# Kernel tuning notes

Measured on AMD Instinct MI355X. Metric: run time of the kernel, lower is better.

## Reference

```python
import jax, jax.numpy as jnp
import numpy as np

B, L, K, S, D, H, C = 32, 256, 50, 16, 128, 4, 128
V, NN, NU, NS = 50000, 100000, 50000, 5000


def mha(q, k, v, in_w, in_b, out_w, out_b, n_heads):
    # PyTorch nn.MultiheadAttention (batch_first, eval mode) semantics.
    d = q.shape[-1]
    hd = d // n_heads
    wq, wk, wv = jnp.split(in_w, 3, axis=0)
    bq, bk, bv = jnp.split(in_b, 3)
    def heads(t):
        return t.reshape(t.shape[:-1] + (n_heads, hd))
    qh = heads(q @ wq.T + bq)
    kh = heads(k @ wk.T + bk)
    vh = heads(v @ wv.T + bv)
    scores = jnp.einsum('...qhd,...khd->...hqk', qh, kh) / jnp.sqrt(jnp.asarray(hd, q.dtype))
    attn = jax.nn.softmax(scores, axis=-1)
    o = jnp.einsum('...hqk,...khd->...qhd', attn, vh)
    o = o.reshape(o.shape[:-2] + (d,))
    return o @ out_w.T + out_b


def conv1d(x, w, b):
    # x: [B, D, L], w: [Cout, D, k]
    y = jax.lax.conv_general_dilated(x, w, (1,), 'VALID', dimension_numbers=('NCH', 'OIH', 'NCH'))
    return y + b[None, :, None]


def meta_path_module(paths, gru_wih, gru_whh, gru_bih, gru_bhh, in_w, in_b, out_w, out_b, ln_g, ln_b):
    # paths: [B, S, T, D] -> [B, D]
    b, s, t, d = paths.shape
    x = paths.reshape(b * s, t, d)
    def step(h, xt):
        gi = xt @ gru_wih.T + gru_bih
        gh = h @ gru_whh.T + gru_bhh
        ir, iz, inn = jnp.split(gi, 3, axis=-1)
        hr, hz, hn = jnp.split(gh, 3, axis=-1)
        r = jax.nn.sigmoid(ir + hr)
        z = jax.nn.sigmoid(iz + hz)
        n = jnp.tanh(inn + r * hn)
        return (1.0 - z) * n + z * h, None
    h0 = jnp.zeros((b * s, d), paths.dtype)
    h, _ = jax.lax.scan(step, h0, jnp.swapaxes(x, 0, 1))
    enc = h.reshape(b, s, d)
    attn = mha(enc, enc, enc, in_w, in_b, out_w, out_b, H)
    y = enc + attn
    mu = jnp.mean(y, -1, keepdims=True)
    var = jnp.var(y, -1, keepdims=True)
    y = (y - mu) / jnp.sqrt(var + 1e-5) * ln_g + ln_b
    return jnp.mean(y, axis=1)


def _forward(word_table, news_table, user_table, source_table,
             wa_in_w, wa_in_b, wa_out_w, wa_out_b,
             conv_w3, conv_b3, conv_w4, conv_b4, conv_w5, conv_b5, fc_w, fc_b,
             nsn_gru_wih, nsn_gru_whh, nsn_gru_bih, nsn_gru_bhh,
             nsn_in_w, nsn_in_b, nsn_out_w, nsn_out_b, nsn_ln_g, nsn_ln_b,
             nun_gru_wih, nun_gru_whh, nun_gru_bih, nun_gru_bhh,
             nun_in_w, nun_in_b, nun_out_w, nun_out_b, nun_ln_g, nun_ln_b,
             mp_w1, mp_b1, mp_w2, mp_b2, cls_w1, cls_b1, cls_w2, cls_b2,
             news_ids, news_word_indices, word_ctx_ids, nsn_src, nsn_end, nun_usr, nun_end):
    # --- fine-grained word embeds: per-token query attending over context news ---
    base = word_table[news_word_indices]              # [B, L, D]
    ctx = news_table[word_ctx_ids]                    # [B, L, K, D] (dominant gather)
    q = base[:, :, None, :]                           # [B, L, 1, D]
    fine = mha(q, ctx, ctx, wa_in_w, wa_in_b, wa_out_w, wa_out_b, H)[:, :, 0, :]
    pad = (news_word_indices == 0)[..., None]
    doc = jnp.where(pad, jnp.zeros((), base.dtype), fine)   # padding_idx=0 -> zeros
    # --- coarse CNN encoder ---
    x = jnp.swapaxes(doc, 1, 2)                       # [B, D, L]
    pooled = [jnp.max(jax.nn.relu(conv1d(x, w, b)), axis=2)
              for w, b in ((conv_w3, conv_b3), (conv_w4, conv_b4), (conv_w5, conv_b5))]
    semantic = jnp.concatenate(pooled, axis=1) @ fc_w.T + fc_b   # [B, D]
    # --- meta-path interaction ---
    start = jnp.broadcast_to(news_table[news_ids][:, None, :], (B, S, D))
    nsn_paths = jnp.stack([start, source_table[nsn_src], news_table[nsn_end]], axis=2)
    nun_paths = jnp.stack([start, user_table[nun_usr], news_table[nun_end]], axis=2)
    nsn_e = meta_path_module(nsn_paths, nsn_gru_wih, nsn_gru_whh, nsn_gru_bih, nsn_gru_bhh,
                             nsn_in_w, nsn_in_b, nsn_out_w, nsn_out_b, nsn_ln_g, nsn_ln_b)
    nun_e = meta_path_module(nun_paths, nun_gru_wih, nun_gru_whh, nun_gru_bih, nun_gru_bhh,
                             nun_in_w, nun_in_b, nun_out_w, nun_out_b, nun_ln_g, nun_ln_b)
    stack = jnp.stack([nsn_e, nun_e], axis=1)         # [B, 2, D]
    sc = jnp.tanh(stack @ mp_w1.T + mp_b1) @ mp_w2.T + mp_b2
    w = jax.nn.softmax(sc, axis=1)
    struct = jnp.sum(stack * w, axis=1)
    comb = jnp.concatenate([semantic, struct], axis=1)
    hcls = jax.nn.relu(comb @ cls_w1.T + cls_b1)
    return hcls @ cls_w2.T + cls_b2                   # [B, 2]


def setup_inputs() -> dict:
    key = jax.random.key(0)
    ks = iter(jax.random.split(key, 80))
    def p(shape):
        return (jax.random.normal(next(ks), shape, jnp.float32) * 0.02)
    inp = {}
    inp['news_ids'] = jax.random.randint(next(ks), (B,), 0, NN)
    inp['news_word_indices'] = jax.random.randint(next(ks), (B, L), 0, V)
    inp['word_ctx_ids'] = jax.random.randint(next(ks), (B, L, K), 0, NN)
    inp['nsn_src'] = jax.random.randint(next(ks), (B, S), 0, NS)
    inp['nsn_end'] = jax.random.randint(next(ks), (B, S), 0, NN)
    inp['nun_usr'] = jax.random.randint(next(ks), (B, S), 0, NU)
    inp['nun_end'] = jax.random.randint(next(ks), (B, S), 0, NN)
    inp['word_table'] = p((V, D)).at[0].set(0.0)
    inp['news_table'] = p((NN, D))
    inp['user_table'] = p((NU, D))
    inp['source_table'] = p((NS, D))
    inp['wa_in_w'] = p((3 * D, D)); inp['wa_in_b'] = p((3 * D,))
    inp['wa_out_w'] = p((D, D)); inp['wa_out_b'] = p((D,))
    for k in (3, 4, 5):
        inp[f'conv_w{k}'] = p((C, D, k)); inp[f'conv_b{k}'] = p((C,))
    inp['fc_w'] = p((D, 3 * C)); inp['fc_b'] = p((D,))
    for pre in ('nsn', 'nun'):
        inp[f'{pre}_gru_wih'] = p((3 * D, D)); inp[f'{pre}_gru_whh'] = p((3 * D, D))
        inp[f'{pre}_gru_bih'] = p((3 * D,)); inp[f'{pre}_gru_bhh'] = p((3 * D,))
        inp[f'{pre}_in_w'] = p((3 * D, D)); inp[f'{pre}_in_b'] = p((3 * D,))
        inp[f'{pre}_out_w'] = p((D, D)); inp[f'{pre}_out_b'] = p((D,))
        inp[f'{pre}_ln_g'] = jnp.ones((D,), jnp.float32); inp[f'{pre}_ln_b'] = jnp.zeros((D,), jnp.float32)
    inp['mp_w1'] = p((D // 2, D)); inp['mp_b1'] = p((D // 2,))
    inp['mp_w2'] = p((1, D // 2)); inp['mp_b2'] = p((1,))
    inp['cls_w1'] = p((D, 2 * D)); inp['cls_b1'] = p((D,))
    inp['cls_w2'] = p((2, D)); inp['cls_b2'] = p((2,))
    return inp


def reference(word_table, news_table, user_table, source_table,
              wa_in_w, wa_in_b, wa_out_w, wa_out_b,
              conv_w3, conv_b3, conv_w4, conv_b4, conv_w5, conv_b5, fc_w, fc_b,
              nsn_gru_wih, nsn_gru_whh, nsn_gru_bih, nsn_gru_bhh,
              nsn_in_w, nsn_in_b, nsn_out_w, nsn_out_b, nsn_ln_g, nsn_ln_b,
              nun_gru_wih, nun_gru_whh, nun_gru_bih, nun_gru_bhh,
              nun_in_w, nun_in_b, nun_out_w, nun_out_b, nun_ln_g, nun_ln_b,
              mp_w1, mp_b1, mp_w2, mp_b2, cls_w1, cls_b1, cls_w2, cls_b2,
              news_ids, news_word_indices, word_ctx_ids, nsn_src, nsn_end, nun_usr, nun_end):
    return _forward(word_table, news_table, user_table, source_table,
                    wa_in_w, wa_in_b, wa_out_w, wa_out_b,
                    conv_w3, conv_b3, conv_w4, conv_b4, conv_w5, conv_b5, fc_w, fc_b,
                    nsn_gru_wih, nsn_gru_whh, nsn_gru_bih, nsn_gru_bhh,
                    nsn_in_w, nsn_in_b, nsn_out_w, nsn_out_b, nsn_ln_g, nsn_ln_b,
                    nun_gru_wih, nun_gru_whh, nun_gru_bih, nun_gru_bhh,
                    nun_in_w, nun_in_b, nun_out_w, nun_out_b, nun_ln_g, nun_ln_b,
                    mp_w1, mp_b1, mp_w2, mp_b2, cls_w1, cls_b1, cls_w2, cls_b2,
                    news_ids, news_word_indices, word_ctx_ids, nsn_src, nsn_end, nun_usr, nun_end)
```

## Files before the change

### kernel.cpp

```cpp
#include <hip/hip_runtime.h>
#include <hip/hip_bf16.h>

#define BB 32
#define LL 256
#define KC 50
#define SS 16
#define DD 128
#define NH 4
#define CC 128
#define VV 50000
#define NNN 100000
#define NUU 50000
#define NSS 5000

typedef __attribute__((ext_vector_type(8))) short bf16x8;
typedef __attribute__((ext_vector_type(8))) unsigned short u16x8;
typedef __attribute__((ext_vector_type(4))) float f32x4;

#define APAD 132

__device__ __forceinline__ float dot4(float4 a, float4 b){
  return a.x*b.x + a.y*b.y + a.z*b.z + a.w*b.w;
}

__device__ __forceinline__ unsigned short f2bf(float f){
  union { float f; unsigned int u; } v; v.f = f;
  unsigned int r = (v.u + 0x7FFFu + ((v.u >> 16) & 1u)) >> 16;
  return (unsigned short)r;
}
__device__ __forceinline__ float bf2f(unsigned short s){
  union { unsigned int u; float f; } v; v.u = ((unsigned int)s) << 16;
  return v.f;
}

__global__ __launch_bounds__(256) void k_prep(
    const float* __restrict__ w3, const float* __restrict__ w4,
    const float* __restrict__ w5,
    const float* __restrict__ wih0, const float* __restrict__ whh0,
    const float* __restrict__ wih1, const float* __restrict__ whh1,
    const float* __restrict__ in_w, const float* __restrict__ out_w,
    const float* __restrict__ inw0, const float* __restrict__ outw0,
    const float* __restrict__ inw1, const float* __restrict__ outw1,
    unsigned short* __restrict__ wb3, unsigned short* __restrict__ wb4,
    unsigned short* __restrict__ wb5, unsigned short* __restrict__ wgb,
    unsigned short* __restrict__ wab, unsigned short* __restrict__ wmh){
  int e = blockIdx.x*256 + threadIdx.x;
  if (e < CC*DD*3){ int c=e/(DD*3), rm=e%(DD*3), d=rm/3, jj=rm%3;
    wb3[((size_t)jj*CC + c)*DD + d] = f2bf(w3[e]); }
  if (e < CC*DD*4){ int c=e/(DD*4), rm=e%(DD*4), d=rm/4, jj=rm%4;
    wb4[((size_t)jj*CC + c)*DD + d] = f2bf(w4[e]); }
  if (e < CC*DD*5){ int c=e/(DD*5), rm=e%(DD*5), d=rm/5, jj=rm%5;
    wb5[((size_t)jj*CC + c)*DD + d] = f2bf(w5[e]); }
  if (e < 384*DD){
    wgb[e]          = f2bf(wih0[e]);
    wgb[49152 + e]  = f2bf(whh0[e]);
    wgb[98304 + e]  = f2bf(wih1[e]);
    wgb[147456 + e] = f2bf(whh1[e]);
    wab[e]          = f2bf(in_w[e]);
  }
  if (e >= 384*DD && e < 512*DD) wab[e] = f2bf(out_w[e - 384*DD]);
  if (e < 512*DD){
    float s0 = (e < 384*DD) ? inw0[e] : outw0[e - 384*DD];
    float s1 = (e < 384*DD) ? inw1[e] : outw1[e - 384*DD];
    wmh[e]                 = f2bf(s0);
    wmh[(size_t)512*DD + e] = f2bf(s1);
  }
}

__global__ __launch_bounds__(256) void k_projkv(
    const float* __restrict__ news, const unsigned short* __restrict__ wkvb,
    const float* __restrict__ in_b, unsigned short* __restrict__ nK,
    unsigned short* __restrict__ nV){
  __shared__ __align__(16) unsigned short Ts[64*APAD];
  const int tid = threadIdx.x;
  const int r0 = blockIdx.x * 64;
  for (int i = tid; i < 64*32; i += 256){
    int row = i >> 5, j = i & 31;
    int gr = r0 + row;
    float4 v = (gr < NNN) ? ((const float4*)(news + (size_t)gr*DD))[j]
                          : make_float4(0.f,0.f,0.f,0.f);
    unsigned short* d = Ts + row*APAD + j*4;
    d[0]=f2bf(v.x); d[1]=f2bf(v.y); d[2]=f2bf(v.z); d[3]=f2bf(v.w);
  }
  __syncthreads();
  const int wave = tid >> 6;
  const int lane = tid & 63;
  const int l15  = lane & 15;
  const int quad = lane >> 4;
  bf16x8 afr[4][4];
  #pragma unroll
  for (int mt=0; mt<4; mt++)
    #pragma unroll
    for (int ks=0; ks<4; ks++)
      afr[mt][ks] = *(const bf16x8*)(Ts + (mt*16 + l15)*APAD + ks*32 + quad*8);
  __syncthreads();
  for (int pass=0; pass<2; pass++){
    unsigned short* outp = pass ? nV : nK;
    #pragma unroll
    for (int t=0; t<2; t++){
      const int n0 = wave*32 + t*16;
      bf16x8 bfr[4];
      #pragma unroll
      for (int ks=0; ks<4; ks++)
        bfr[ks] = *(const bf16x8*)(wkvb + (size_t)(pass*128 + n0 + l15)*DD + ks*32 + quad*8);
      const float bias = in_b[128 + pass*128 + n0 + l15];
      #pragma unroll
      for (int mt=0; mt<4; mt++){
        f32x4 acc = {0.f,0.f,0.f,0.f};
        #pragma unroll
        for (int ks=0; ks<4; ks++)
          acc = __builtin_amdgcn_mfma_f32_16x16x32_bf16(afr[mt][ks], bfr[ks], acc, 0,0,0);
        const int col = n0 + l15;
        const int rb  = mt*16 + quad*4;
        #pragma unroll
        for (int r=0;r<4;r++)
          Ts[(rb + r)*APAD + col] = f2bf(acc[r] + bias);
      }
    }
    __syncthreads();
    for (int c = tid; c < 64*32; c += 256){
      int row = c >> 5, col4 = (c & 31) * 4;
      int gr = r0 + row;
      if (gr < NNN)
        *(unsigned long long*)(outp + (size_t)gr*128 + col4) =
            *(const unsigned long long*)(Ts + row*APAD + col4);
    }
    __syncthreads();
  }
}

__global__ __launch_bounds__(64) void k_qh(
    const float* __restrict__ word_table, const int* __restrict__ widx,
    const unsigned short* __restrict__ wqb, const float* __restrict__ in_b,
    float* __restrict__ qh){
  const int lane = threadIdx.x;
  const int l15 = lane & 15, quad = lane >> 4;
  const int p0 = blockIdx.x * 16;
  const int row = widx[p0 + l15];
  const float* src = word_table + (size_t)row*DD + quad*8;
  bf16x8 afr[4];
  #pragma unroll
  for (int ks=0; ks<4; ks++){
    float4 v0 = *(const float4*)(src + ks*32);
    float4 v1 = *(const float4*)(src + ks*32 + 4);
    bf16x8 a;
    a[0]=(short)f2bf(v0.x); a[1]=(short)f2bf(v0.y); a[2]=(short)f2bf(v0.z); a[3]=(short)f2bf(v0.w);
    a[4]=(short)f2bf(v1.x); a[5]=(short)f2bf(v1.y); a[6]=(short)f2bf(v1.z); a[7]=(short)f2bf(v1.w);
    afr[ks] = a;
  }
  #pragma unroll
  for (int nt=0; nt<8; nt++){
    const int n0 = nt*16;
    bf16x8 bfr[4];
    #pragma unroll
    for (int ks=0; ks<4; ks++)
      bfr[ks] = *(const bf16x8*)(wqb + (size_t)(n0+l15)*DD + ks*32 + quad*8);
    const float bias = in_b[n0 + l15];
    f32x4 acc = {0.f,0.f,0.f,0.f};
    #pragma unroll
    for (int ks=0; ks<4; ks++)
      acc = __builtin_amdgcn_mfma_f32_16x16x32_bf16(afr[ks], bfr[ks], acc, 0,0,0);
    #pragma unroll
    for (int r=0;r<4;r++){
      int m = quad*4 + r;
      qh[(size_t)(p0+m)*DD + n0 + l15] = acc[r] + bias;
    }
  }
}

__global__ __launch_bounds__(64) void k_attn(
    const float* __restrict__ qh, const unsigned short* __restrict__ nK,
    const unsigned short* __restrict__ nV, const int* __restrict__ ctx_ids,
    unsigned short* __restrict__ o_out){
  const int p = blockIdx.x;
  const int lane = threadIdx.x;
  const int r = lane >> 4;
  const int g = lane & 15;
  const int h = g >> 2;
  __shared__ int ids[52];
  __shared__ float sc[NH][52];
  if (lane < KC) ids[lane] = ctx_ids[(size_t)p*KC + lane];
  float qv[8];
  {
    const float4* qp = (const float4*)(qh + (size_t)p*DD + g*8);
    float4 q0 = qp[0], q1 = qp[1];
    qv[0]=q0.x; qv[1]=q0.y; qv[2]=q0.z; qv[3]=q0.w;
    qv[4]=q1.x; qv[5]=q1.y; qv[6]=q1.z; qv[7]=q1.w;
  }
  __syncthreads();
  for (int kb=0; kb<13; kb++){
    int k2 = kb*4 + r;
    int row = ids[(k2 < KC) ? k2 : 0];
    u16x8 kv = *(const u16x8*)(nK + (size_t)row*DD + g*8);
    float pr = 0.f;
    #pragma unroll
    for (int j=0;j<8;j++) pr += qv[j]*bf2f(kv[j]);
    pr += __shfl_xor(pr, 1, 64);
    pr += __shfl_xor(pr, 2, 64);
    if ((g & 3) == 0 && k2 < KC) sc[h][k2] = pr;
  }
  __syncthreads();
  {
    const int hh = lane >> 4, kc = lane & 15;
    const float scale = 0.17677669529663687f;
    float mx = -1e30f;
    #pragma unroll
    for (int q4=0;q4<4;q4++){ int k2=kc+q4*16; if (k2<KC) mx = fmaxf(mx, sc[hh][k2]); }
    mx = fmaxf(mx, __shfl_xor(mx, 1, 64));
    mx = fmaxf(mx, __shfl_xor(mx, 2, 64));
    mx = fmaxf(mx, __shfl_xor(mx, 4, 64));
    mx = fmaxf(mx, __shfl_xor(mx, 8, 64));
    float sm = 0.f;
    float ev[4];
    #pragma unroll
    for (int q4=0;q4<4;q4++){
      int k2=kc+q4*16;
      ev[q4] = (k2<KC) ? __expf((sc[hh][k2]-mx)*scale) : 0.f;
      sm += ev[q4];
    }
    sm += __shfl_xor(sm, 1, 64);
    sm += __shfl_xor(sm, 2, 64);
    sm += __shfl_xor(sm, 4, 64);
    sm += __shfl_xor(sm, 8, 64);
    float inv = 1.f/sm;
    #pragma unroll
    for (int q4=0;q4<4;q4++){ int k2=kc+q4*16; if (k2<KC) sc[hh][k2] = ev[q4]*inv; }
  }
  __syncthreads();
  float acc[8];
  #pragma unroll
  for (int j=0;j<8;j++) acc[j]=0.f;
  for (int kb=0; kb<13; kb++){
    int k2 = kb*4 + r;
    int row = ids[(k2 < KC) ? k2 : 0];
    float w = (k2 < KC) ? sc[h][k2] : 0.f;
    u16x8 vv = *(const u16x8*)(nV + (size_t)row*DD + g*8);
    #pragma unroll
    for (int j=0;j<8;j++) acc[j] += w*bf2f(vv[j]);
  }
  #pragma unroll
  for (int j=0;j<8;j++){
    acc[j] += __shfl_xor(acc[j], 16, 64);
    acc[j] += __shfl_xor(acc[j], 32, 64);
  }
  if (r == 0){
    u16x8 o;
    #pragma unroll
    for (int j=0;j<8;j++) o[j] = f2bf(acc[j]);
    *(u16x8*)(o_out + (size_t)p*DD + g*8) = o;
  }
}

__global__ __launch_bounds__(64) void k_wo(
    const unsigned short* __restrict__ o_attn, const int* __restrict__ widx,
    const unsigned short* __restrict__ wob, const float* __restrict__ out_b,
    unsigned short* __restrict__ doc){
  const int lane = threadIdx.x;
  const int l15 = lane & 15, quad = lane >> 4;
  const int p0 = blockIdx.x * 16;
  bf16x8 afr[4];
  #pragma unroll
  for (int ks=0; ks<4; ks++)
    afr[ks] = *(const bf16x8*)(o_attn + (size_t)(p0+l15)*DD + ks*32 + quad*8);
  int msk[4];
  #pragma unroll
  for (int r=0;r<4;r++) msk[r] = widx[p0 + quad*4 + r];
  #pragma unroll
  for (int nt=0; nt<8; nt++){
    const int n0 = nt*16;
    bf16x8 bfr[4];
    #pragma unroll
    for (int ks=0; ks<4; ks++)
      bfr[ks] = *(const bf16x8*)(wob + (size_t)(n0+l15)*DD + ks*32 + quad*8);
    const float bias = out_b[n0 + l15];
    f32x4 acc = {0.f,0.f,0.f,0.f};
    #pragma unroll
    for (int ks=0; ks<4; ks++)
      acc = __builtin_amdgcn_mfma_f32_16x16x32_bf16(afr[ks], bfr[ks], acc, 0,0,0);
    #pragma unroll
    for (int r=0;r<4;r++){
      int m = quad*4 + r;
      doc[(size_t)(p0+m)*DD + n0 + l15] = (msk[r] == 0) ? (unsigned short)0
                                                        : f2bf(acc[r] + bias);
    }
  }
}

#define CROWS 68
#define CPAD 136
__global__ __launch_bounds__(256) void k_conv(
    const unsigned short* __restrict__ doc, const unsigned short* __restrict__ wb3,
    const unsigned short* __restrict__ wb4, const unsigned short* __restrict__ wb5,
    float* __restrict__ convp){
  __shared__ __align__(16) char smem[CROWS*CPAD*2];
  unsigned short* ds = (unsigned short*)smem;
  float* smf = (float*)smem;
  const int blk = blockIdx.x;
  const int chunk = blk & 3;
  const int j = (blk >> 2) % 3;
  const int b = blk / 12;
  const int kk = 3 + j;
  const int T = LL - kk + 1;
  const int t0 = chunk * 64;
  const int nrows = 64 + kk - 1;
  const unsigned short* wb = (j==0) ? wb3 : (j==1) ? wb4 : wb5;
  const int tid = threadIdx.x;
  for (int i = tid; i < nrows*16; i += 256){
    int row = i >> 4, q8 = i & 15;
    int gt = t0 + row;
    u16x8 v = (u16x8){0,0,0,0,0,0,0,0};
    if (gt < LL) v = *(const u16x8*)(doc + ((size_t)b*LL + gt)*DD + q8*8);
    *(u16x8*)(ds + row*CPAD + q8*8) = v;
  }
  __syncthreads();
  const int wave = tid >> 6;
  const int lane = tid & 63;
  const int l15  = lane & 15;
  const int quad = lane >> 4;
  f32x4 acc[8];
  #pragma unroll
  for (int nt=0;nt<8;nt++) acc[nt] = (f32x4){0.f,0.f,0.f,0.f};
  for (int jj=0; jj<kk; jj++){
    #pragma unroll
    for (int ks=0; ks<4; ks++){
      bf16x8 af = *(const bf16x8*)(ds + (wave*16 + l15 + jj)*CPAD + ks*32 + quad*8);
      #pragma unroll
      for (int nt=0; nt<8; nt++){
        bf16x8 bf = *(const bf16x8*)(wb + ((size_t)jj*CC + nt*16 + l15)*DD + ks*32 + quad*8);
        acc[nt] = __builtin_amdgcn_mfma_f32_16x16x32_bf16(af, bf, acc[nt], 0,0,0);
      }
    }
  }
  __syncthreads();
  #pragma unroll
  for (int nt=0; nt<8; nt++){
    float mx = -1e30f;
    #pragma unroll
    for (int r=0;r<4;r++){
      int t = t0 + wave*16 + quad*4 + r;
      mx = fmaxf(mx, (t < T) ? acc[nt][r] : -1e30f);
    }
    mx = fmaxf(mx, __shfl_xor(mx, 16, 64));
    mx = fmaxf(mx, __shfl_xor(mx, 32, 64));
    if (quad == 0) smf[wave*128 + nt*16 + l15] = mx;
  }
  __syncthreads();
  if (tid < 128){
    float m4 = fmaxf(fmaxf(smf[tid], smf[128+tid]), fmaxf(smf[256+tid], smf[384+tid]));
    convp[(((size_t)b*3 + j)*4 + chunk)*CC + tid] = m4;
  }
}

#define GSTR 392
__global__ __launch_bounds__(256) void k_gru(
    const float* __restrict__ news_table, const float* __restrict__ user_table,
    const float* __restrict__ source_table,
    const int* __restrict__ news_ids, const int* __restrict__ nsn_src,
    const int* __restrict__ nsn_end, const int* __restrict__ nun_usr,
    const int* __restrict__ nun_end,
    const unsigned short* __restrict__ wgb,
    const float* __restrict__ bih0, const float* __restrict__ bhh0,
    const float* __restrict__ bih1, const float* __restrict__ bhh1,
    float* __restrict__ enc){
  __shared__ __align__(16) unsigned short xs[16][CPAD];
  __shared__ __align__(16) unsigned short hs[16][CPAD];
  __shared__ float hf[8][128];
  __shared__ float gi[8][GSTR];
  __shared__ float gh[8][GSTR];
  const int blk = blockIdx.x;
  const int m  = blk >> 6;
  const int b  = (blk >> 1) & 31;
  const int s0 = (blk & 1) * 8;
  const int tid = threadIdx.x;
  const int wave = tid >> 6, lane = tid & 63, l15 = lane & 15, quad = lane >> 4;
  const unsigned short* Wih = wgb + (size_t)m*2*384*DD;
  const unsigned short* Whh = Wih + 384*DD;
  const float* bih = m ? bih1 : bih0;
  const float* bhh = m ? bhh1 : bhh0;
  for (int i=tid;i<16*CPAD;i+=256){ (&xs[0][0])[i]=0; (&hs[0][0])[i]=0; }
  for (int i=tid;i<8*128;i+=256) (&hf[0][0])[i]=0.f;
  __syncthreads();
  for (int t=0;t<3;t++){
    {
      int s = tid >> 5, j = tid & 31;
      int row; const float* tab;
      if (t==0){ row = news_ids[b]; tab = news_table; }
      else if (t==1){ row = m ? nun_usr[b*SS+s0+s] : nsn_src[b*SS+s0+s];
                      tab = m ? user_table : source_table; }
      else { row = m ? nun_end[b*SS+s0+s] : nsn_end[b*SS+s0+s]; tab = news_table; }
      float4 v = ((const float4*)(tab + (size_t)row*DD))[j];
      unsigned short* dp = &xs[s][j*4];
      dp[0]=f2bf(v.x); dp[1]=f2bf(v.y); dp[2]=f2bf(v.z); dp[3]=f2bf(v.w);
    }
    __syncthreads();
    bf16x8 ax[4], ah[4];
    #pragma unroll
    for (int ks=0;ks<4;ks++){
      ax[ks] = *(const bf16x8*)&xs[l15][ks*32+quad*8];
      ah[ks] = *(const bf16x8*)&hs[l15][ks*32+quad*8];
    }
    #pragma unroll
    for (int nt=0;nt<6;nt++){
      const int n0 = wave*96 + nt*16;
      f32x4 ga = {0.f,0.f,0.f,0.f}, ha = {0.f,0.f,0.f,0.f};
      #pragma unroll
      for (int ks=0;ks<4;ks++){
        bf16x8 bi = *(const bf16x8*)(Wih + (size_t)(n0+l15)*DD + ks*32+quad*8);
        ga = __builtin_amdgcn_mfma_f32_16x16x32_bf16(ax[ks], bi, ga, 0,0,0);
        bf16x8 bh = *(const bf16x8*)(Whh + (size_t)(n0+l15)*DD + ks*32+quad*8);
        ha = __builtin_amdgcn_mfma_f32_16x16x32_bf16(ah[ks], bh, ha, 0,0,0);
      }
      if (quad < 2){
        #pragma unroll
        for (int r=0;r<4;r++){
          gi[quad*4+r][n0+l15] = ga[r];
          gh[quad*4+r][n0+l15] = ha[r];
        }
      }
    }
    __syncthreads();
    #pragma unroll
    for (int k=0;k<4;k++){
      int it = tid + k*256;
      int s = it >> 7, g = it & 127;
      float rr = 1.f/(1.f+__expf(-(gi[s][g] + gh[s][g] + bih[g] + bhh[g])));
      float zz = 1.f/(1.f+__expf(-(gi[s][128+g] + gh[s][128+g] + bih[128+g] + bhh[128+g])));
      float nn = tanhf(gi[s][256+g] + bih[256+g] + rr*(gh[s][256+g] + bhh[256+g]));
      float hnew = (1.f-zz)*nn + zz*hf[s][g];
      hf[s][g] = hnew;
      hs[s][g] = f2bf(hnew);
    }
    __syncthreads();
  }
  {
    int s = tid >> 5, j = tid & 31;
    float4 v = ((const float4*)hf[s])[j];
    ((float4*)(enc + (((size_t)m*BB + b)*SS + (s0+s))*DD))[j] = v;
  }
}

#define MPAD 136
__global__ __launch_bounds__(256) void k_metamha(
    const float* __restrict__ enc,
    const unsigned short* __restrict__ wmh,
    const float* __restrict__ inb0, const float* __restrict__ outb0,
    const float* __restrict__ lng0, const float* __restrict__ lnb0,
    const float* __restrict__ inb1, const float* __restrict__ outb1,
    const float* __restrict__ lng1, const float* __restrict__ lnb1,
    float* __restrict__ meta_e){
  const int m = blockIdx.x >> 5;
  const int b = blockIdx.x & 31;
  const int tid = threadIdx.x;
  const int wave = tid >> 6, lane = tid & 63, l15 = lane & 15, quad = lane >> 4;
  const unsigned short* W = wmh + (size_t)m*512*DD;
  const float* in_b  = m ? inb1 : inb0;
  const float* out_b = m ? outb1 : outb0;
  const float* lng   = m ? lng1 : lng0;
  const float* lnb   = m ? lnb1 : lnb0;

  __shared__ __align__(16) unsigned short ebf[16][MPAD];
  __shared__ __align__(16) unsigned short qb[16][MPAD];
  __shared__ __align__(16) unsigned short kb[16][MPAD];
  __shared__ __align__(16) unsigned short ob[16][MPAD];
  __shared__ float vf[16][128];
  __shared__ float er[16][132];
  __shared__ float at[NH][16][16];
  __shared__ float mu[16], rs[16];
  __shared__ float part[2][128];

  const float* esrc = enc + ((size_t)m*BB + b)*SS*DD;
  for (int i = tid; i < 16*32; i += 256){
    int s = i >> 5, j = i & 31;
    float4 v = ((const float4*)esrc)[i];
    ((float4*)er[s])[j] = v;
    unsigned short* dp = &ebf[s][j*4];
    dp[0]=f2bf(v.x); dp[1]=f2bf(v.y); dp[2]=f2bf(v.z); dp[3]=f2bf(v.w);
  }
  __syncthreads();
  {
    bf16x8 ax[4];
    #pragma unroll
    for (int ks=0;ks<4;ks++) ax[ks] = *(const bf16x8*)&ebf[l15][ks*32+quad*8];
    #pragma unroll
    for (int nt=0; nt<6; nt++){
      const int n0 = wave*96 + nt*16;
      f32x4 acc = {0.f,0.f,0.f,0.f};
      #pragma unroll
      for (int ks=0;ks<4;ks++){
        bf16x8 bw = *(const bf16x8*)(W + (size_t)(n0+l15)*DD + ks*32+quad*8);
        acc = __builtin_amdgcn_mfma_f32_16x16x32_bf16(ax[ks], bw, acc, 0,0,0);
      }
      const float bias = in_b[n0+l15];
      const int col = n0 + l15;
      #pragma unroll
      for (int r=0;r<4;r++){
        int row = quad*4+r;
        float val = acc[r] + bias;
        if (n0 < 128)      qb[row][col]       = f2bf(val);
        else if (n0 < 256) kb[row][col-128]   = f2bf(val);
        else               vf[row][col-256]   = val;
      }
    }
  }
  __syncthreads();
  {
    const int h = wave;
    bf16x8 aq = *(const bf16x8*)&qb[l15][h*32 + quad*8];
    bf16x8 ak = *(const bf16x8*)&kb[l15][h*32 + quad*8];
    f32x4 z = {0.f,0.f,0.f,0.f};
    f32x4 acc = __builtin_amdgcn_mfma_f32_16x16x32_bf16(aq, ak, z, 0,0,0);
    #pragma unroll
    for (int r=0;r<4;r++)
      at[h][quad*4+r][l15] = acc[r] * 0.17677669529663687f;
  }
  __syncthreads();
  if (tid < 64){
    int h = tid>>4, qi = tid&15;
    float mx=-1e30f;
    #pragma unroll
    for (int ki=0;ki<16;ki++) mx = fmaxf(mx, at[h][qi][ki]);
    float sm=0.f;
    float ee[16];
    #pragma unroll
    for (int ki=0;ki<16;ki++){ ee[ki]=__expf(at[h][qi][ki]-mx); sm+=ee[ki]; }
    float inv=1.f/sm;
    #pragma unroll
    for (int ki=0;ki<16;ki++) at[h][qi][ki]=ee[ki]*inv;
  }
  __syncthreads();
  {
    int c = tid & 127, h = c >> 5;
    int sBase = (tid >> 7) * 8;
    #pragma unroll
    for (int s=0;s<8;s++){
      float acc=0.f;
      #pragma unroll
      for (int ki=0;ki<16;ki++) acc += at[h][sBase+s][ki]*vf[ki][c];
      ob[sBase+s][c] = f2bf(acc);
    }
  }
  __syncthreads();
  {
    bf16x8 ao[4];
    #pragma unroll
    for (int ks=0;ks<4;ks++) ao[ks] = *(const bf16x8*)&ob[l15][ks*32+quad*8];
    #pragma unroll
    for (int nt=0; nt<2; nt++){
      const int n0 = wave*32 + nt*16;
      f32x4 acc = {0.f,0.f,0.f,0.f};
      #pragma unroll
      for (int ks=0;ks<4;ks++){
        bf16x8 bw = *(const bf16x8*)(W + (size_t)(384 + n0+l15)*DD + ks*32+quad*8);
        acc = __builtin_amdgcn_mfma_f32_16x16x32_bf16(ao[ks], bw, acc, 0,0,0);
      }
      const float bias = out_b[n0+l15];
      const int col = n0 + l15;
      #pragma unroll
      for (int r=0;r<4;r++){
        int row = quad*4 + r;
        er[row][col] += acc[r] + bias;
      }
    }
  }
  __syncthreads();
  {
    int row = tid >> 4, i = tid & 15;
    const float* yr = &er[row][i*8];
    float s1=0.f, s2=0.f;
    #pragma unroll
    for (int j2=0;j2<8;j2++){ float y=yr[j2]; s1+=y; s2+=y*y; }
    #pragma unroll
    for (int msk=1; msk<16; msk<<=1){
      s1 += __shfl_xor(s1, msk, 64);
      s2 += __shfl_xor(s2, msk, 64);
    }
    if (i==0){
      float mean = s1*(1.f/128.f);
      mu[row]=mean;
      rs[row]=rsqrtf(s2*(1.f/128.f) - mean*mean + 1e-5f);
    }
  }
  __syncthreads();
  {
    int c = tid & 127, half = tid >> 7;
    float g = lng[c], bb2 = lnb[c];
    float acc=0.f;
    #pragma unroll
    for (int s=0;s<8;s++){
      int ss = half*8+s;
      acc += (er[ss][c]-mu[ss])*rs[ss]*g + bb2;
    }
    part[half][c]=acc;
  }
  __syncthreads();
  if (tid < 128)
    meta_e[((size_t)m*BB+b)*DD + tid] = (part[0][tid]+part[1][tid]) * (1.f/16.f);
}

__global__ __launch_bounds__(128) void k_final(
    const float* __restrict__ convp,
    const float* __restrict__ cb3, const float* __restrict__ cb4,
    const float* __restrict__ cb5,
    const float* __restrict__ fc_w, const float* __restrict__ fc_b,
    const float* __restrict__ meta_e,
    const float* __restrict__ mp_w1, const float* __restrict__ mp_b1,
    const float* __restrict__ mp_w2, const float* __restrict__ mp_b2,
    const float* __restrict__ cls_w1, const float* __restrict__ cls_b1,
    const float* __restrict__ cls_w2, const float* __restrict__ cls_b2,
    float* __restrict__ out){
  const int b = blockIdx.x;
  const int c = threadIdx.x;
  __shared__ float pooled[384];
  __shared__ float comb[256];
  __shared__ float hcls[128];
  __shared__ float tt[2][64];
  __shared__ float wsc[2];
  for (int idx=c; idx<384; idx+=128){
    int j = idx >> 7, cc2 = idx & 127;
    const float* base = convp + (((size_t)b*3 + j)*4)*CC + cc2;
    float mx = -1e30f;
    for (int ci=0;ci<4;ci++) mx = fmaxf(mx, base[ci*CC]);
    const float* cb = (j==0)?cb3:(j==1)?cb4:cb5;
    pooled[idx] = fmaxf(mx + cb[cc2], 0.f);
  }
  __syncthreads();
  {
    float acc = fc_b[c];
    const float* wr = fc_w + (size_t)c*384;
    for (int i=0;i<384;i++) acc += pooled[i]*wr[i];
    comb[c] = acc;
  }
  if (c < 64){
    for (int m=0;m<2;m++){
      const float* ev = meta_e + ((size_t)m*BB+b)*DD;
      float acc = mp_b1[c];
      const float* wr = mp_w1 + (size_t)c*DD;
      for (int i=0;i<DD;i++) acc += ev[i]*wr[i];
      tt[m][c] = tanhf(acc);
    }
  }
  __syncthreads();
  if (c == 0){
    float s0 = mp_b2[0], s1 = mp_b2[0];
    for (int j=0;j<64;j++){ s0 += tt[0][j]*mp_w2[j]; s1 += tt[1][j]*mp_w2[j]; }
    float mx = fmaxf(s0,s1);
    float e0 = __expf(s0-mx), e1 = __expf(s1-mx);
    wsc[0] = e0/(e0+e1); wsc[1] = e1/(e0+e1);
  }
  __syncthreads();
  comb[128+c] = wsc[0]*meta_e[((size_t)b)*DD + c]
              + wsc[1]*meta_e[((size_t)(BB+b))*DD + c];
  __syncthreads();
  {
    float acc = cls_b1[c];
    const float* wr = cls_w1 + (size_t)c*256;
    for (int i=0;i<256;i++) acc += comb[i]*wr[i];
    hcls[c] = fmaxf(acc, 0.f);
  }
  __syncthreads();
  if (c < 2){
    float acc = cls_b2[c];
    const float* wr = cls_w2 + (size_t)c*DD;
    for (int i=0;i<DD;i++) acc += hcls[i]*wr[i];
    out[b*2 + c] = acc;
  }
}

extern "C" void kernel_launch(void* const* d_in, const int* in_sizes, int n_in,
                              void* d_out, int out_size, void* d_ws, size_t ws_size,
                              hipStream_t stream){
  const int* news_ids = (const int*)d_in[0];
  const int* nwi      = (const int*)d_in[1];
  const int* ctx_ids  = (const int*)d_in[2];
  const int* nsn_src  = (const int*)d_in[3];
  const int* nsn_end  = (const int*)d_in[4];
  const int* nun_usr  = (const int*)d_in[5];
  const int* nun_end  = (const int*)d_in[6];
  const float* word_table   = (const float*)d_in[7];
  const float* news_table   = (const float*)d_in[8];
  const float* user_table   = (const float*)d_in[9];
  const float* source_table = (const float*)d_in[10];
  const float* wa_in_w  = (const float*)d_in[11];
  const float* wa_in_b  = (const float*)d_in[12];
  const float* wa_out_w = (const float*)d_in[13];
  const float* wa_out_b = (const float*)d_in[14];
  const float* conv_w3 = (const float*)d_in[15];
  const float* conv_b3 = (const float*)d_in[16];
  const float* conv_w4 = (const float*)d_in[17];
  const float* conv_b4 = (const float*)d_in[18];
  const float* conv_w5 = (const float*)d_in[19];
  const float* conv_b5 = (const float*)d_in[20];
  const float* fc_w = (const float*)d_in[21];
  const float* fc_b = (const float*)d_in[22];
  const float* wih0 = (const float*)d_in[23];
  const float* whh0 = (const float*)d_in[24];
  const float* bih0 = (const float*)d_in[25];
  const float* bhh0 = (const float*)d_in[26];
  const float* inw0 = (const float*)d_in[27];
  const float* inb0 = (const float*)d_in[28];
  const float* outw0 = (const float*)d_in[29];
  const float* outb0 = (const float*)d_in[30];
  const float* lng0 = (const float*)d_in[31];
  const float* lnb0 = (const float*)d_in[32];
  const float* wih1 = (const float*)d_in[33];
  const float* whh1 = (const float*)d_in[34];
  const float* bih1 = (const float*)d_in[35];
  const float* bhh1 = (const float*)d_in[36];
  const float* inw1 = (const float*)d_in[37];
  const float* inb1 = (const float*)d_in[38];
  const float* outw1 = (const float*)d_in[39];
  const float* outb1 = (const float*)d_in[40];
  const float* lng1 = (const float*)d_in[41];
  const float* lnb1 = (const float*)d_in[42];
  const float* mp_w1 = (const float*)d_in[43];
  const float* mp_b1 = (const float*)d_in[44];
  const float* mp_w2 = (const float*)d_in[45];
  const float* mp_b2 = (const float*)d_in[46];
  const float* cls_w1 = (const float*)d_in[47];
  const float* cls_b1 = (const float*)d_in[48];
  const float* cls_w2 = (const float*)d_in[49];
  const float* cls_b2 = (const float*)d_in[50];

  char* wsb = (char*)d_ws;
  unsigned short* nK = (unsigned short*)wsb;
  unsigned short* nV = nK + (size_t)NNN*DD;
  unsigned short* wb3 = nV + (size_t)NNN*DD;
  unsigned short* wb4 = wb3 + (size_t)CC*DD*3;
  unsigned short* wb5 = wb4 + (size_t)CC*DD*4;
  unsigned short* wgb = wb5 + (size_t)CC*DD*5;
  unsigned short* wab = wgb + (size_t)4*384*DD;
  unsigned short* wmh = wab + (size_t)512*DD;
  float* qh     = (float*)(wmh + (size_t)2*512*DD);
  unsigned short* o_at = (unsigned short*)(qh + (size_t)BB*LL*DD);
  unsigned short* doc  = (unsigned short*)((float*)o_at + (size_t)BB*LL*DD);
  float* convp  = (float*)doc + (size_t)BB*LL*DD;
  float* enc    = convp + BB*3*4*CC;
  float* meta_e = enc + (size_t)2*BB*SS*DD;
  const size_t need_bytes = (size_t)((char*)(meta_e + 2*BB*DD) - wsb);
  if (ws_size < need_bytes) return;

  const unsigned short* wqb  = wab;
  const unsigned short* wkvb = wab + (size_t)128*DD;
  const unsigned short* wob  = wab + (size_t)384*DD;

  k_prep<<<dim3(320), dim3(256), 0, stream>>>(conv_w3, conv_w4, conv_w5,
      wih0, whh0, wih1, whh1, wa_in_w, wa_out_w,
      inw0, outw0, inw1, outw1,
      wb3, wb4, wb5, wgb, wab, wmh);
  k_projkv<<<dim3((NNN+63)/64), dim3(256), 0, stream>>>(news_table, wkvb, wa_in_b, nK, nV);
  k_qh<<<dim3(BB*LL/16), dim3(64), 0, stream>>>(word_table, nwi, wqb, wa_in_b, qh);
  k_attn<<<dim3(BB*LL), dim3(64), 0, stream>>>(qh, nK, nV, ctx_ids, o_at);
  k_wo<<<dim3(BB*LL/16), dim3(64), 0, stream>>>(o_at, nwi, wob, wa_out_b, doc);
  k_conv<<<dim3(BB*3*4), dim3(256), 0, stream>>>(doc, wb3, wb4, wb5, convp);
  k_gru<<<dim3(128), dim3(256), 0, stream>>>(news_table, user_table, source_table,
      news_ids, nsn_src, nsn_end, nun_usr, nun_end,
      wgb, bih0, bhh0, bih1, bhh1, enc);
  k_metamha<<<dim3(64), dim3(256), 0, stream>>>(enc, wmh,
      inb0, outb0, lng0, lnb0,
      inb1, outb1, lng1, lnb1, meta_e);
  k_final<<<dim3(BB), dim3(128), 0, stream>>>(convp, conv_b3, conv_b4, conv_b5,
      fc_w, fc_b, meta_e, mp_w1, mp_b1, mp_w2, mp_b2,
      cls_w1, cls_b1, cls_w2, cls_b2, (float*)d_out);
}
```

Before: 362.5 us.

## Restructure K/V projection to 16-row tiles without shared-memory staging

```diff
diff --git a/kernel.cpp b/kernel.cpp
--- a/kernel.cpp
+++ b/kernel.cpp
@@ -71,61 +71,43 @@
     const float* __restrict__ news, const unsigned short* __restrict__ wkvb,
     const float* __restrict__ in_b, unsigned short* __restrict__ nK,
     unsigned short* __restrict__ nV){
-  __shared__ __align__(16) unsigned short Ts[64*APAD];
-  const int tid = threadIdx.x;
-  const int r0 = blockIdx.x * 64;
-  for (int i = tid; i < 64*32; i += 256){
-    int row = i >> 5, j = i & 31;
-    int gr = r0 + row;
-    float4 v = (gr < NNN) ? ((const float4*)(news + (size_t)gr*DD))[j]
-                          : make_float4(0.f,0.f,0.f,0.f);
-    unsigned short* d = Ts + row*APAD + j*4;
-    d[0]=f2bf(v.x); d[1]=f2bf(v.y); d[2]=f2bf(v.z); d[3]=f2bf(v.w);
-  }
-  __syncthreads();
+  const int tid  = threadIdx.x;
   const int wave = tid >> 6;
   const int lane = tid & 63;
   const int l15  = lane & 15;
   const int quad = lane >> 4;
-  bf16x8 afr[4][4];
-  #pragma unroll
-  for (int mt=0; mt<4; mt++)
+  const int r0   = blockIdx.x * 16;
+  const int nw0  = wave * 64;
+
+  const float* src = news + (size_t)(r0 + l15)*DD + quad*8;
+  bf16x8 afr[4];
+  #pragma unroll
+  for (int ks=0; ks<4; ks++){
+    float4 v0 = *(const float4*)(src + ks*32);
+    float4 v1 = *(const float4*)(src + ks*32 + 4);
+    bf16x8 a;
+    a[0]=(short)f2bf(v0.x); a[1]=(short)f2bf(v0.y); a[2]=(short)f2bf(v0.z); a[3]=(short)f2bf(v0.w);
+    a[4]=(short)f2bf(v1.x); a[5]=(short)f2bf(v1.y); a[6]=(short)f2bf(v1.z); a[7]=(short)f2bf(v1.w);
+    afr[ks] = a;
+  }
+  unsigned short* outp = (nw0 < 128) ? nK : nV;
+  const int cbase = nw0 & 127;
+  #pragma unroll
+  for (int nt=0; nt<4; nt++){
+    const int n0 = nw0 + nt*16;
+    bf16x8 bfr[4];
     #pragma unroll
     for (int ks=0; ks<4; ks++)
-      afr[mt][ks] = *(const bf16x8*)(Ts + (mt*16 + l15)*APAD + ks*32 + quad*8);
-  __syncthreads();
-  for (int pass=0; pass<2; pass++){
-    unsigned short* outp = pass ? nV : nK;
-    #pragma unroll
-    for (int t=0; t<2; t++){
-      const int n0 = wave*32 + t*16;
-      bf16x8 bfr[4];
-      #pragma unroll
-      for (int ks=0; ks<4; ks++)
-        bfr[ks] = *(const bf16x8*)(wkvb + (size_t)(pass*128 + n0 + l15)*DD + ks*32 + quad*8);
-      const float bias = in_b[128 + pass*128 + n0 + l15];
-      #pragma unroll
-      for (int mt=0; mt<4; mt++){
-        f32x4 acc = {0.f,0.f,0.f,0.f};
-        #pragma unroll
-        for (int ks=0; ks<4; ks++)
-          acc = __builtin_amdgcn_mfma_f32_16x16x32_bf16(afr[mt][ks], bfr[ks], acc, 0,0,0);
-        const int col = n0 + l15;
-        const int rb  = mt*16 + quad*4;
-        #pragma unroll
-        for (int r=0;r<4;r++)
-          Ts[(rb + r)*APAD + col] = f2bf(acc[r] + bias);
-      }
-    }
-    __syncthreads();
-    for (int c = tid; c < 64*32; c += 256){
-      int row = c >> 5, col4 = (c & 31) * 4;
-      int gr = r0 + row;
-      if (gr < NNN)
-        *(unsigned long long*)(outp + (size_t)gr*128 + col4) =
-            *(const unsigned long long*)(Ts + row*APAD + col4);
-    }
-    __syncthreads();
+      bfr[ks] = *(const bf16x8*)(wkvb + (size_t)(n0 + l15)*DD + ks*32 + quad*8);
+    const float bias = in_b[128 + n0 + l15];
+    f32x4 acc = {0.f,0.f,0.f,0.f};
+    #pragma unroll
+    for (int ks=0; ks<4; ks++)
+      acc = __builtin_amdgcn_mfma_f32_16x16x32_bf16(afr[ks], bfr[ks], acc, 0,0,0);
+    const int c = cbase + nt*16 + l15;
+    #pragma unroll
+    for (int r=0;r<4;r++)
+      outp[(size_t)(r0 + quad*4 + r)*DD + c] = f2bf(acc[r] + bias);
   }
 }
 
@@ -747,7 +729,7 @@
       wih0, whh0, wih1, whh1, wa_in_w, wa_out_w,
       inw0, outw0, inw1, outw1,
       wb3, wb4, wb5, wgb, wab, wmh);
-  k_projkv<<<dim3((NNN+63)/64), dim3(256), 0, stream>>>(news_table, wkvb, wa_in_b, nK, nV);
+  k_projkv<<<dim3(NNN/16), dim3(256), 0, stream>>>(news_table, wkvb, wa_in_b, nK, nV);
   k_qh<<<dim3(BB*LL/16), dim3(64), 0, stream>>>(word_table, nwi, wqb, wa_in_b, qh);
   k_attn<<<dim3(BB*LL), dim3(64), 0, stream>>>(qh, nK, nV, ctx_ids, o_at);
   k_wo<<<dim3(BB*LL/16), dim3(64), 0, stream>>>(o_at, nwi, wob, wa_out_b, doc);
```

Result: slower. 404.7 us (+11.6%).
